# Kernel tuning notes

Measured on AMD Instinct MI355X. Metric: run time of the kernel, lower is better.

Reference implementation:

```python
import jax, jax.numpy as jnp
import numpy as np

C = 768
H = 12
B = 4
T = 16
K = 196


def _ln(x, g, b, eps=1e-5):
    mu = jnp.mean(x, axis=-1, keepdims=True)
    var = jnp.mean(jnp.square(x - mu), axis=-1, keepdims=True)
    return (x - mu) / jnp.sqrt(var + eps) * g + b


def _mha(x, Wq, bq, Wk, bk, Wv, bv):
    # x: [b, n, c]; standard multi-head attention, scale = head_dim**-0.5
    b, n, c = x.shape
    hd = c // H
    scale = hd ** -0.5
    def heads(y):
        return y.reshape(b, n, H, hd).transpose(0, 2, 1, 3)  # b h n d
    q = heads(x @ Wq + bq)
    k = heads(x @ Wk + bk)
    v = heads(x @ Wv + bv)
    a = jax.nn.softmax(jnp.einsum('bhqd,bhkd->bhqk', q, k) * scale, axis=-1)
    o = jnp.einsum('bhqk,bhkd->bhqd', a, v)
    return o.transpose(0, 2, 1, 3).reshape(b, n, c)


def setup_inputs() -> dict:
    key = jax.random.key(0)
    ks = jax.random.split(key, 8)
    M = T * K + 1
    w = lambda k, shape: jax.random.normal(k, shape, dtype=jnp.float32) * 0.02
    return {
        'x': jax.random.normal(ks[0], (B, M, C), dtype=jnp.float32),
        'ln1_g': jnp.ones((C,), jnp.float32), 'ln1_b': jnp.zeros((C,), jnp.float32),
        'tln_g': jnp.ones((C,), jnp.float32), 'tln_b': jnp.zeros((C,), jnp.float32),
        'ln2_g': jnp.ones((C,), jnp.float32), 'ln2_b': jnp.zeros((C,), jnp.float32),
        'Ws': w(ks[1], (4, C, C)), 'bs': jnp.zeros((4, C), jnp.float32),
        'Wt': w(ks[2], (9, C, C)), 'bt': jnp.zeros((9, C), jnp.float32),
        'Wtp': w(ks[3], (3, C, C)), 'btp': jnp.zeros((3, C), jnp.float32),
        'Wfc': w(ks[4], (C, C)), 'bfc': jnp.zeros((C,), jnp.float32),
        'W1': w(ks[5], (C, 4 * C)), 'b1': jnp.zeros((4 * C,), jnp.float32),
        'W2': w(ks[6], (4 * C, C)), 'b2': jnp.zeros((C,), jnp.float32),
        'T': T, 'K': K,
    }


def reference(x, ln1_g, ln1_b, tln_g, tln_b, ln2_g, ln2_b, Ws, bs, Wt, bt, Wtp, btp, Wfc, bfc, W1, b1, W2, b2, T, K):
    Bsz, M, Cd = x.shape
    t1, t2 = T // 4, T // 2
    # ---- temporal branch: 'b (k t) c -> (b k) t c' ----
    xt = x[:, 1:].reshape(Bsz * K, T, Cd)
    h = _ln(xt, tln_g, tln_b)
    # three windowed temporal scales
    o4 = _mha(h[:, T - t1:], Wt[0], bt[0], Wt[1], bt[1], Wt[2], bt[2])
    o8 = _mha(h[:, t2:], Wt[3], bt[3], Wt[4], bt[4], Wt[5], bt[5])
    o16 = _mha(h, Wt[6], bt[6], Wt[7], bt[7], Wt[8], bt[8])
    o4 = o4 @ Wtp[0] + btp[0]
    o8 = o8.at[:, t1:].set(0.5 * o8[:, t1:] + 0.5 * o4)
    o8 = o8 @ Wtp[1] + btp[1]
    o16 = o16.at[:, t2:].set(0.5 * o16[:, t2:] + 0.5 * o8)
    o16 = o16 @ Wtp[2] + btp[2]
    res_temporal = o16.reshape(Bsz, K * T, Cd)  # '(b k) t c -> b (k t) c'
    xt2 = res_temporal @ Wfc + bfc + x[:, 1:]
    # ---- spatial branch: 'b (k t) c -> (b t) k c' with cls prepended ----
    init_cls = x[:, :1]  # [B,1,C]
    cls = jnp.broadcast_to(init_cls, (Bsz, T, Cd)).reshape(Bsz * T, 1, Cd)
    xs = xt2.reshape(Bsz, K, T, Cd).transpose(0, 2, 1, 3).reshape(Bsz * T, K, Cd)
    xs = jnp.concatenate([cls, xs], axis=1)  # [(B T), K+1, C]
    hs = _ln(xs, ln1_g, ln1_b)
    os_ = _mha(hs, Ws[0], bs[0], Ws[1], bs[1], Ws[2], bs[2]) @ Ws[3] + bs[3]
    cls_out = os_[:, 0].reshape(Bsz, T, Cd).mean(axis=1, keepdims=True)
    res_spatial = os_[:, 1:].reshape(Bsz, T, K, Cd).transpose(0, 2, 1, 3).reshape(Bsz, K * T, Cd)
    xn = jnp.concatenate([init_cls, xt2], axis=1) + jnp.concatenate([cls_out, res_spatial], axis=1)
    # ---- MLP ----
    h2 = _ln(xn, ln2_g, ln2_b)
    mlp = jax.nn.gelu(h2 @ W1 + b1, approximate=False) @ W2 + b2
    return xn + mlp
```

## Files before the change

kernel.cpp:

```cpp
#include <hip/hip_runtime.h>

typedef unsigned short u16;
typedef unsigned int   u32;
typedef __attribute__((ext_vector_type(8))) __bf16 bf16x8;
typedef __attribute__((ext_vector_type(4))) float  f32x4;
typedef __attribute__((ext_vector_type(4))) u16    u16x4;

#define DEV __device__ __forceinline__

DEV float bf2f(u16 u){ union { u32 i; float f; } x; x.i = ((u32)u) << 16; return x.f; }
DEV u16 f2bf(float f){ union { float f; u32 i; } x; x.f = f;
  u32 r = x.i + 0x7fffu + ((x.i >> 16) & 1u); return (u16)(r >> 16); }

DEV void gload16(const void* g, void* l){
  __builtin_amdgcn_global_load_lds((const __attribute__((address_space(1))) void*)g,
                                   (__attribute__((address_space(3))) void*)l, 16, 0, 0);
}

__global__ __launch_bounds__(256)
void twt_k(const float* __restrict__ src, u16* __restrict__ dst, int R, int C){
  __shared__ float t[32][33];
  int tx = threadIdx.x & 31, ty = threadIdx.x >> 5;
  int c0 = blockIdx.x * 32, r0 = blockIdx.y * 32;
  #pragma unroll
  for (int i = 0; i < 4; i++)
    t[ty + i*8][tx] = src[(size_t)(r0 + ty + i*8) * C + c0 + tx];
  __syncthreads();
  #pragma unroll
  for (int i = 0; i < 4; i++)
    dst[(size_t)(c0 + ty + i*8) * R + r0 + tx] = f2bf(t[tx][ty + i*8]);
}

__global__ __launch_bounds__(256)
void twt17_k(const float* __restrict__ Ws, const float* __restrict__ Wt,
             const float* __restrict__ Wtp, const float* __restrict__ Wfc,
             u16* __restrict__ dst){
  __shared__ float t[32][33];
  int z = blockIdx.z;
  const float* src = (z < 4)  ? Ws  + (size_t)z * 589824
                   : (z < 13) ? Wt  + (size_t)(z-4) * 589824
                   : (z < 16) ? Wtp + (size_t)(z-13) * 589824
                   : Wfc;
  u16* d = dst + (size_t)z * 589824;
  int tx = threadIdx.x & 31, ty = threadIdx.x >> 5;
  int c0 = blockIdx.x * 32, r0 = blockIdx.y * 32;
  #pragma unroll
  for (int i = 0; i < 4; i++)
    t[ty + i*8][tx] = src[(size_t)(r0 + ty + i*8) * 768 + c0 + tx];
  __syncthreads();
  #pragma unroll
  for (int i = 0; i < 4; i++)
    d[(size_t)(c0 + ty + i*8) * 768 + r0 + tx] = f2bf(t[tx][ty + i*8]);
}

__global__ __launch_bounds__(256)
void cvt_k(const float* __restrict__ src, u16* __restrict__ dst){
  int i = (blockIdx.x * 256 + threadIdx.x) * 4;
  float4 f = *(const float4*)(src + i);
  u16x4 p; p[0] = f2bf(f.x); p[1] = f2bf(f.y); p[2] = f2bf(f.z); p[3] = f2bf(f.w);
  *(u16x4*)(dst + i) = p;
}

__global__ __launch_bounds__(256)
void bprep_k(const float* __restrict__ btp2, const u16* __restrict__ WfcT,
             const float* __restrict__ bfc, float* __restrict__ bprime,
             float* __restrict__ zb){
  int lane = threadIdx.x & 63;
  int n = blockIdx.x * 4 + (threadIdx.x >> 6);
  const u16* wr = WfcT + (size_t)n * 768 + lane * 12;
  const float* br = btp2 + lane * 12;
  float acc = 0.f;
  #pragma unroll
  for (int i = 0; i < 3; i++){
    u16x4 w = *(const u16x4*)(wr + i * 4);
    float4 b = *(const float4*)(br + i * 4);
    acc += bf2f(w[0]) * b.x + bf2f(w[1]) * b.y + bf2f(w[2]) * b.z + bf2f(w[3]) * b.w;
  }
  #pragma unroll
  for (int off = 32; off; off >>= 1) acc += __shfl_xor(acc, off);
  if (lane == 0){ bprime[n] = acc + bfc[n]; zb[n] = 0.f; }
}

__global__ void fillz_k(u32* __restrict__ p, long n){
  long i = (long)blockIdx.x * 256 + threadIdx.x;
  long stride = (long)gridDim.x * 256;
  for (; i < n; i += stride) p[i] = 0;
}

template<int GM>
__global__ __launch_bounds__(256)
void ln_k(const float* __restrict__ f0, const u16* __restrict__ b0_,
          const float* __restrict__ gw, const float* __restrict__ bw,
          u16* __restrict__ out){
  int lane = threadIdx.x & 63;
  int tok = blockIdx.x * 4 + (threadIdx.x >> 6);
  const float* fsrc = nullptr; const u16* bsrc = nullptr;
  bool bfp = false;
  if constexpr (GM == 0){
    int b = tok / 3136, m = tok - b * 3136;
    fsrc = f0 + ((size_t)b * 3137 + 1 + m) * 768;
  } else if constexpr (GM == 1){
    int s = tok / 197, j = tok - s * 197;
    int b = s >> 4, t = s & 15;
    if (j == 0) fsrc = f0 + (size_t)b * 3137 * 768;
    else { bfp = true; bsrc = b0_ + ((size_t)b * 3136 + (size_t)(j - 1) * 16 + t) * 768; }
  } else {
    fsrc = f0 + (size_t)tok * 768;
  }
  float v[12]; float s1 = 0.f, s2 = 0.f;
  if (!bfp){
    #pragma unroll
    for (int i = 0; i < 3; i++){
      float4 f = *(const float4*)(fsrc + i * 256 + lane * 4);
      v[i*4+0] = f.x; v[i*4+1] = f.y; v[i*4+2] = f.z; v[i*4+3] = f.w;
    }
  } else {
    #pragma unroll
    for (int i = 0; i < 3; i++){
      u16x4 p = *(const u16x4*)(bsrc + i * 256 + lane * 4);
      v[i*4+0] = bf2f(p[0]); v[i*4+1] = bf2f(p[1]); v[i*4+2] = bf2f(p[2]); v[i*4+3] = bf2f(p[3]);
    }
  }
  #pragma unroll
  for (int i = 0; i < 12; i++){ s1 += v[i]; s2 += v[i]*v[i]; }
  #pragma unroll
  for (int off = 32; off; off >>= 1){ s1 += __shfl_xor(s1, off); s2 += __shfl_xor(s2, off); }
  float mu = s1 * (1.f/768.f);
  float rstd = rsqrtf(s2 * (1.f/768.f) - mu*mu + 1e-5f);
  #pragma unroll
  for (int i = 0; i < 3; i++){
    int c = i * 256 + lane * 4;
    float4 g4 = *(const float4*)(gw + c);
    float4 b4 = *(const float4*)(bw + c);
    u16x4 pk;
    pk[0] = f2bf((v[i*4+0]-mu)*rstd*g4.x + b4.x);
    pk[1] = f2bf((v[i*4+1]-mu)*rstd*g4.y + b4.y);
    pk[2] = f2bf((v[i*4+2]-mu)*rstd*g4.z + b4.z);
    pk[3] = f2bf((v[i*4+3]-mu)*rstd*g4.w + b4.w);
    *(u16x4*)(out + (size_t)tok * 768 + c) = pk;
  }
}

template<int MODE, int BIG>
__global__ __launch_bounds__(BIG ? 512 : 256, 4)
void gemm_k(const u16* __restrict__ A, const u16* __restrict__ Bw,
            const float* __restrict__ bias, void* out,
            const void* aux1, void* aux2, int nbx,
            int M, int K, int lda, int ldo,
            int aTs, int aTf, int at0, int oTs, int oTf, int ot0){
  constexpr int BM = BIG ? 256 : 128;
  constexpr int THREADS = BIG ? 512 : 256;
  __shared__ u16 lA[2][BM * 32];
  __shared__ u16 lB[2][128 * 32];
  const int tid = threadIdx.x;

  const int nwg = (int)gridDim.x;
  int id = (int)blockIdx.x;
  int qc = nwg >> 3, rc = nwg & 7;
  int xcd = id & 7, off = id >> 3;
  int wg = (xcd < rc ? xcd * (qc + 1) : rc * (qc + 1) + (xcd - rc) * qc) + off;
  int by = wg / nbx;
  int bx = wg - by * nbx;
  const int m0 = by * BM, n0 = bx * 128;

  const int lane = tid & 63, widx = tid >> 6;
  const int g = lane >> 4, r16 = lane & 15;
  const int wm = widx >> 1, wn = widx & 1;

  const u16* ga0; const u16* ga1; const u16* gb0; const u16* gb1 = nullptr;
  u32 loA0, loA1, loB0, loB1 = 0;
  {
    int li = tid;
    int ar = m0 + (li >> 2); if (ar > M - 1) ar = M - 1;
    ar = (ar / aTs) * aTf + at0 + (ar % aTs);
    ga0 = A + (size_t)ar * lda + (li & 3) * 8;
    loA0 = li * 8;
    li = tid + THREADS;
    ar = m0 + (li >> 2); if (ar > M - 1) ar = M - 1;
    ar = (ar / aTs) * aTf + at0 + (ar % aTs);
    ga1 = A + (size_t)ar * lda + (li & 3) * 8;
    loA1 = li * 8;
    gb0 = Bw + (size_t)(n0 + (tid >> 2)) * K + (tid & 3) * 8;
    loB0 = tid * 8;
    if constexpr (!BIG){
      int lj = tid + 256;
      gb1 = Bw + (size_t)(n0 + (lj >> 2)) * K + (lj & 3) * 8;
      loB1 = lj * 8;
    }
  }

  const f32x4 vz = {0.f, 0.f, 0.f, 0.f};
  f32x4 acc[4][4];
  #pragma unroll
  for (int i = 0; i < 4; i++)
    #pragma unroll
    for (int j = 0; j < 4; j++) acc[i][j] = vz;

  const int kiter = K >> 5;

  gload16(ga0, &lA[0][loA0]);
  gload16(ga1, &lA[0][loA1]);
  gload16(gb0, &lB[0][loB0]);
  if constexpr (!BIG) gload16(gb1, &lB[0][loB1]);
  ga0 += 32; ga1 += 32; gb0 += 32;
  if constexpr (!BIG) gb1 += 32;
  __syncthreads();

  for (int kt = 0; kt < kiter; ++kt){
    const int cur = kt & 1;
    if (kt + 1 < kiter){
      const int nxt = cur ^ 1;
      gload16(ga0, &lA[nxt][loA0]);
      gload16(ga1, &lA[nxt][loA1]);
      gload16(gb0, &lB[nxt][loB0]);
      if constexpr (!BIG) gload16(gb1, &lB[nxt][loB1]);
      ga0 += 32; ga1 += 32; gb0 += 32;
      if constexpr (!BIG) gb1 += 32;
    }
    bf16x8 af[4], bfr[4];
    #pragma unroll
    for (int i = 0; i < 4; i++){
      af[i]  = *(const bf16x8*)(&lA[cur][(wm * 64 + i * 16 + r16) * 32 + g * 8]);
      bfr[i] = *(const bf16x8*)(&lB[cur][(wn * 64 + i * 16 + r16) * 32 + g * 8]);
    }
    #pragma unroll
    for (int i = 0; i < 4; i++)
      #pragma unroll
      for (int j = 0; j < 4; j++)
        acc[i][j] = __builtin_amdgcn_mfma_f32_16x16x32_bf16(af[i], bfr[j], acc[i][j], 0, 0, 0);
    __syncthreads();
  }

  #pragma unroll
  for (int i = 0; i < 4; i++){
    const int lrow = wm * 64 + i * 16 + g * 4;
    #pragma unroll
    for (int j = 0; j < 4; j++){
      const int Cg = n0 + wn * 64 + j * 16 + r16;
      const float b0 = bias[Cg];
      float vv[4];
      #pragma unroll
      for (int r = 0; r < 4; r++) vv[r] = acc[i][j][r] + b0;

      if constexpr (MODE == 8){
        int mat = Cg / 768, c0 = Cg - mat * 768;
        if (mat < 2){
          #pragma unroll
          for (int r = 0; r < 4; r++){
            int R = m0 + lrow + r;
            if (R < M)
              ((u16*)out)[(size_t)mat * ot0 * 768 + (size_t)R * 768 + c0] = f2bf(vv[r]);
          }
        } else {
          int R0 = m0 + lrow;
          if (R0 < M){
            int seq_ = R0 / oTs, t0 = R0 - seq_ * oTs;
            u16x4 pk;
            #pragma unroll
            for (int r = 0; r < 4; r++) pk[r] = f2bf(vv[r]);
            *(u16x4*)((u16*)aux2 +
              ((size_t)(seq_ * 12 + (c0 >> 6)) * 64 + (c0 & 63)) * ldo + t0) = pk;
          }
        }
      } else if constexpr (MODE == 9){
        int mat = Cg / 768, c0 = Cg - mat * 768;
        if (mat < 2){
          #pragma unroll
          for (int r = 0; r < 4; r++){
            int R = m0 + lrow + r;
            if (R < M)
              ((u16*)out)[(size_t)mat * ot0 * 768 + (size_t)R * 768 + c0] = f2bf(vv[r]);
          }
        } else {
          int R0 = m0 + lrow;
          if (R0 < M){
            int s_ = R0 / 197, j0 = R0 - s_ * 197;
            if (j0 <= 193){
              u16x4 pk;
              #pragma unroll
              for (int r = 0; r < 4; r++) pk[r] = f2bf(vv[r]);
              *(u16x4*)((u16*)aux2 +
                ((size_t)(s_ * 12 + (c0 >> 6)) * 64 + (c0 & 63)) * 224 + j0 + (s_ & 3)) = pk;
            } else {
              #pragma unroll
              for (int r = 0; r < 4; r++){
                int R = R0 + r;
                if (R < M){
                  int s2 = R / 197, j2 = R - s2 * 197;
                  ((u16*)aux2)[((size_t)(s2 * 12 + (c0 >> 6)) * 64 + (c0 & 63)) * 224
                               + j2 + (s2 & 3)] = f2bf(vv[r]);
                }
              }
            }
          }
        }
      } else {
        #pragma unroll
        for (int r = 0; r < 4; r++){
          const int R = m0 + lrow + r;
          if (R >= M) continue;
          float val = vv[r];
          if constexpr (MODE == 0){
            ((u16*)out)[(size_t)R * ldo + Cg] = f2bf(val);
          } else if constexpr (MODE == 1){
            int Ro = (R / oTs) * oTf + ot0 + (R % oTs);
            u16* po = (u16*)out + (size_t)Ro * ldo + Cg;
            *po = f2bf(0.5f * val + 0.5f * bf2f(*po));
          } else if constexpr (MODE == 2){
            int b_ = R / 3136, m_ = R - b_ * 3136;
            ((u16*)out)[(size_t)R * 768 + Cg] =
                f2bf(val + ((const float*)aux1)[((size_t)b_ * 3137 + 1 + m_) * 768 + Cg]);
          } else if constexpr (MODE == 3){
            int s_ = R / 197, j_ = R - s_ * 197;
            if (j_ == 0){
              ((float*)aux2)[(size_t)s_ * 768 + Cg] = val;
            } else {
              int b_ = s_ >> 4, t_ = s_ & 15, m_ = (j_ - 1) * 16 + t_;
              ((float*)out)[((size_t)b_ * 3137 + 1 + m_) * 768 + Cg] =
                  val + bf2f(((const u16*)aux1)[((size_t)b_ * 3136 + m_) * 768 + Cg]);
            }
          } else if constexpr (MODE == 4){
            float c = val * (0.7978845608f + 0.0356774081f * val * val);
            float e2 = __expf(2.f * fabsf(c));
            float th = __builtin_copysignf(1.f - 2.f / (e2 + 1.f), c);
            ((u16*)out)[(size_t)R * ldo + Cg] = f2bf(0.5f * val * (1.f + th));
          } else if constexpr (MODE == 5){
            ((float*)out)[(size_t)R * 768 + Cg] = val + ((const float*)aux1)[(size_t)R * 768 + Cg];
          }
        }
      }
    }
  }
}

template<int TS, int TSPAD>
__global__ __launch_bounds__(256)
void tattn_k(const u16* __restrict__ q, const u16* __restrict__ k,
             const u16* __restrict__ vt, u16* __restrict__ o){
  const int lane = threadIdx.x & 63;
  const int g = lane >> 4, r16 = lane & 15;
  int p = blockIdx.x * 4 + (threadIdx.x >> 6);
  int seq = p / 12, h = p - seq * 12;

  int trow = (TS < 16 && r16 >= TS) ? TS - 1 : r16;
  size_t qko = (size_t)(seq * TS + trow) * 768 + h * 64 + g * 8;
  bf16x8 ak0 = *(const bf16x8*)(k + qko);
  bf16x8 ak1 = *(const bf16x8*)(k + qko + 32);
  bf16x8 bq0 = *(const bf16x8*)(q + qko);
  bf16x8 bq1 = *(const bf16x8*)(q + qko + 32);

  f32x4 s = {0.f, 0.f, 0.f, 0.f};
  s = __builtin_amdgcn_mfma_f32_16x16x32_bf16(ak0, bq0, s, 0, 0, 0);
  s = __builtin_amdgcn_mfma_f32_16x16x32_bf16(ak1, bq1, s, 0, 0, 0);

  const float C = 0.125f * 1.44269504089f;
  float pv[4]; float mx = -3e38f;
  #pragma unroll
  for (int r = 0; r < 4; r++){
    float x = (g * 4 + r < TS) ? s[r] : -3e38f;
    pv[r] = x; mx = fmaxf(mx, x);
  }
  mx = fmaxf(mx, __shfl_xor(mx, 16));
  mx = fmaxf(mx, __shfl_xor(mx, 32));
  float sum = 0.f;
  #pragma unroll
  for (int r = 0; r < 4; r++){ pv[r] = exp2f((pv[r] - mx) * C); sum += pv[r]; }
  sum += __shfl_xor(sum, 16);
  sum += __shfl_xor(sum, 32);
  float inv = 1.f / sum;
  #pragma unroll
  for (int r = 0; r < 4; r++) pv[r] *= inv;

  u32 w0 = (u32)f2bf(pv[0]) | ((u32)f2bf(pv[1]) << 16);
  u32 w1 = (u32)f2bf(pv[2]) | ((u32)f2bf(pv[3]) << 16);
  int a0 = ((g * 2) * 16 + r16) * 4;
  int a1 = ((g * 2 + 1) * 16 + r16) * 4;
  u32 msk = (g < 2) ? 0xFFFFFFFFu : 0u;
  union { u32 w[4]; bf16x8 v; } pa;
  pa.w[0] = msk & (u32)__builtin_amdgcn_ds_bpermute(a0, (int)w0);
  pa.w[1] = msk & (u32)__builtin_amdgcn_ds_bpermute(a0, (int)w1);
  pa.w[2] = msk & (u32)__builtin_amdgcn_ds_bpermute(a1, (int)w0);
  pa.w[3] = msk & (u32)__builtin_amdgcn_ds_bpermute(a1, (int)w1);

  const u16* vb = vt + ((size_t)(seq * 12 + h) * 64) * TSPAD;
  const f32x4 vz = {0.f, 0.f, 0.f, 0.f};
  f32x4 oc[4];
  #pragma unroll
  for (int dt = 0; dt < 4; ++dt){
    bf16x8 bv = *(const bf16x8*)(vb + (size_t)(dt * 16 + r16) * TSPAD + g * 8);
    oc[dt] = __builtin_amdgcn_mfma_f32_16x16x32_bf16(pa.v, bv, vz, 0, 0, 0);
  }
  #pragma unroll
  for (int rr = 0; rr < 4; ++rr){
    int qr = g * 4 + rr;
    if (qr < TS){
      size_t ob = (size_t)(seq * TS + qr) * 768 + h * 64 + r16;
      #pragma unroll
      for (int dt = 0; dt < 4; ++dt)
        o[ob + dt * 16] = f2bf(oc[dt][rr]);
    }
  }
}

__global__ __launch_bounds__(256)
void sattn_k(const u16* __restrict__ qs, const u16* __restrict__ ks,
             const u16* __restrict__ vt, u16* __restrict__ o){
  __shared__ u16 PlAll[4][16 * 224];
  const int wid = threadIdx.x >> 6;
  u16* Pl = PlAll[wid];
  const int lane = threadIdx.x & 63;
  const int g = lane >> 4, r16 = lane & 15;
  int gi = blockIdx.x * 4 + wid;
  int chunk = gi % 13; int sh_ = gi / 13;
  int h = sh_ % 12, s = sh_ / 12;
  const int shft = s & 3;
  const float sc_l2e = 0.125f * 1.44269504089f;

  #pragma unroll
  for (int i = 0; i < 4; i++){
    Pl[(i * 4 + g) * 224 + 208 + r16] = 0;
    if (r16 < 4) Pl[(i * 4 + g) * 224 + r16] = 0;
  }

  int q0 = chunk * 16;
  int qrow = q0 + r16; if (qrow > 196) qrow = 196;
  const u16* qp = qs + ((size_t)(s * 197 + qrow)) * 768 + h * 64 + g * 8;
  bf16x8 aq0 = *(const bf16x8*)qp;
  bf16x8 aq1 = *(const bf16x8*)(qp + 32);

  f32x4 scv[13];
  #pragma unroll
  for (int jt = 0; jt < 13; ++jt){
    int krow = jt * 16 + r16; if (krow > 196) krow = 196;
    const u16* kp = ks + ((size_t)(s * 197 + krow)) * 768 + h * 64 + g * 8;
    bf16x8 b0 = *(const bf16x8*)kp;
    bf16x8 b1 = *(const bf16x8*)(kp + 32);
    f32x4 z = {0.f, 0.f, 0.f, 0.f};
    z = __builtin_amdgcn_mfma_f32_16x16x32_bf16(aq0, b0, z, 0, 0, 0);
    z = __builtin_amdgcn_mfma_f32_16x16x32_bf16(aq1, b1, z, 0, 0, 0);
    scv[jt] = z;
  }
  float mrow[4] = {-3e38f, -3e38f, -3e38f, -3e38f};
  #pragma unroll
  for (int jt = 0; jt < 13; ++jt)
    #pragma unroll
    for (int r = 0; r < 4; r++){
      float x = (jt * 16 + r16 < 197) ? scv[jt][r] : -3e38f;
      scv[jt][r] = x;
      mrow[r] = fmaxf(mrow[r], x);
    }
  #pragma unroll
  for (int off = 1; off < 16; off <<= 1)
    #pragma unroll
    for (int r = 0; r < 4; r++) mrow[r] = fmaxf(mrow[r], __shfl_xor(mrow[r], off));
  float srow[4] = {0.f, 0.f, 0.f, 0.f};
  #pragma unroll
  for (int jt = 0; jt < 13; ++jt)
    #pragma unroll
    for (int r = 0; r < 4; r++){
      float e = exp2f((scv[jt][r] - mrow[r]) * sc_l2e);
      scv[jt][r] = e;
      srow[r] += e;
    }
  #pragma unroll
  for (int off = 1; off < 16; off <<= 1)
    #pragma unroll
    for (int r = 0; r < 4; r++) srow[r] += __shfl_xor(srow[r], off);
  float inv[4];
  #pragma unroll
  for (int r = 0; r < 4; r++) inv[r] = 1.f / srow[r];
  #pragma unroll
  for (int jt = 0; jt < 13; ++jt)
    #pragma unroll
    for (int r = 0; r < 4; r++)
      Pl[(g * 4 + r) * 224 + jt * 16 + r16 + shft] = f2bf(scv[jt][r] * inv[r]);
  __syncthreads();
  const u16* vbase = vt + ((size_t)(s * 12 + h) * 64) * 224;
  f32x4 oc[4]; const f32x4 vz = {0.f,0.f,0.f,0.f};
  #pragma unroll
  for (int dt = 0; dt < 4; dt++) oc[dt] = vz;
  #pragma unroll
  for (int ks2 = 0; ks2 < 7; ++ks2){
    bf16x8 ap = *(const bf16x8*)(Pl + r16 * 224 + ks2 * 32 + g * 8);
    #pragma unroll
    for (int dt = 0; dt < 4; ++dt){
      const u16* vp = vbase + ((size_t)(dt * 16 + r16)) * 224 + ks2 * 32 + g * 8;
      bf16x8 bv = *(const bf16x8*)vp;
      oc[dt] = __builtin_amdgcn_mfma_f32_16x16x32_bf16(ap, bv, oc[dt], 0, 0, 0);
    }
  }
  #pragma unroll
  for (int dt = 0; dt < 4; ++dt)
    #pragma unroll
    for (int r = 0; r < 4; r++){
      int qr2 = q0 + g * 4 + r;
      if (qr2 < 197)
        o[((size_t)(s * 197 + qr2)) * 768 + h * 64 + dt * 16 + r16] = f2bf(oc[dt][r]);
    }
}

__global__ __launch_bounds__(256)
void clsfin_k(const float* __restrict__ x, const float* __restrict__ cb, float* __restrict__ xn){
  int b = blockIdx.x;
  int c = blockIdx.y * 256 + threadIdx.x;
  float s = 0.f;
  #pragma unroll
  for (int t = 0; t < 16; t++) s += cb[((size_t)(b * 16 + t)) * 768 + c];
  xn[(size_t)b * 3137 * 768 + c] = x[(size_t)b * 3137 * 768 + c] + s * (1.f / 16.f);
}

extern "C" void kernel_launch(void* const* d_in, const int* in_sizes, int n_in,
                              void* d_out, int out_size, void* d_ws, size_t ws_size,
                              hipStream_t stream){
  (void)in_sizes; (void)n_in; (void)out_size;
  const float* x    = (const float*)d_in[0];
  const float* ln1g = (const float*)d_in[1];
  const float* ln1b = (const float*)d_in[2];
  const float* tlng = (const float*)d_in[3];
  const float* tlnb = (const float*)d_in[4];
  const float* ln2g = (const float*)d_in[5];
  const float* ln2b = (const float*)d_in[6];
  const float* Ws   = (const float*)d_in[7];
  const float* bs   = (const float*)d_in[8];
  const float* Wt   = (const float*)d_in[9];
  const float* bt   = (const float*)d_in[10];
  const float* Wtp  = (const float*)d_in[11];
  const float* btp  = (const float*)d_in[12];
  const float* Wfc  = (const float*)d_in[13];
  const float* bfc  = (const float*)d_in[14];
  const float* W1   = (const float*)d_in[15];
  const float* b1   = (const float*)d_in[16];
  const float* W2   = (const float*)d_in[17];
  const float* b2   = (const float*)d_in[18];
  float* out = (float*)d_out;

  constexpr size_t MiB = 1048576;
  constexpr size_t C2  = 589824;
  constexpr size_t W_BYTES = (17 * C2 + 2 * 2359296) * 2;
  constexpr size_t NEED = W_BYTES + 143 * MiB;
  if (ws_size < NEED) return;

  char* wsb  = (char*)d_ws;
  u16*  wbuf = (u16*)wsb;
  u16*  W1T  = wbuf + 17 * C2;
  u16*  W2T  = W1T + (size_t)3072 * 768;
  char* A0   = wsb + W_BYTES;

  u16*  ht  = (u16*)(A0 + 0   * MiB);
  u16*  qk  = (u16*)(A0 + 20  * MiB);
  u16*  vtb = (u16*)(A0 + 58  * MiB);
  u16*  o16 = (u16*)(A0 + 86  * MiB);
  u16*  o8  = (u16*)(A0 + 105 * MiB);
  u16*  o4  = (u16*)(A0 + 115 * MiB);
  u16*  xt2 = (u16*)(A0 + 105 * MiB);
  float* xn = (float*)(A0 + 20 * MiB);
  u16*  wtp2b = (u16*)(A0 + 132 * MiB);
  u16*  WpT   = (u16*)(A0 + 134 * MiB);
  float* bprime = (float*)(A0 + 136 * MiB);
  float* zb     = bprime + 1024;
  float* clsb = (float*)(A0 + 142 * MiB);
  u16*  hs  = ht;  u16* osb = ht; u16* h2 = ht;
  u16*  a1  = (u16*)(A0 + 58 * MiB);

  twt17_k<<<dim3(24, 24, 17), 256, 0, stream>>>(Ws, Wt, Wtp, Wfc, wbuf);
  twt_k<<<dim3(96, 24), 256, 0, stream>>>(W1, W1T, 768, 3072);
  twt_k<<<dim3(24, 96), 256, 0, stream>>>(W2, W2T, 3072, 768);
  cvt_k<<<576, 256, 0, stream>>>(Wtp + 2 * 589824, wtp2b);
  bprep_k<<<192, 256, 0, stream>>>(btp + 1536, wbuf + 16*C2, bfc, bprime, zb);
  gemm_k<0,0><<<36, 256, 0, stream>>>(wbuf + 16*C2, wtp2b, zb, WpT, nullptr, nullptr, 6, 768, 768, 768, 768, 1,1,0, 1,1,0);

  ln_k<0><<<3136, 256, 0, stream>>>(x, nullptr, tlng, tlnb, ht);

  gemm_k<8,1><<<49*18, 512, 0, stream>>>(ht, wbuf + 10*C2, bt + 6*768, qk, nullptr, vtb, 18, 12544, 768, 768, 24, 1,1,0, 16,1,12544);
  tattn_k<16,24><<<2352, 256, 0, stream>>>(qk, qk + (size_t)12544*768, vtb, o16);

  gemm_k<8,0><<<49*18, 256, 0, stream>>>(ht, wbuf +  7*C2, bt + 3*768, qk, nullptr, vtb, 18, 6272, 768, 768, 16, 8,16,8, 8,1,6272);
  tattn_k< 8,16><<<2352, 256, 0, stream>>>(qk, qk + (size_t)6272*768, vtb, o8);

  gemm_k<8,0><<<25*18, 256, 0, stream>>>(ht, wbuf +  4*C2, bt + 0*768, qk, nullptr, vtb, 18, 3136, 768, 768, 16, 4,16,12, 4,1,3136);
  tattn_k< 4,16><<<2352, 256, 0, stream>>>(qk, qk + (size_t)3136*768, vtb, o4);

  gemm_k<1,0><<<25*6, 256, 0, stream>>>(o4,  wbuf + 13*C2, btp + 0,   o8,  nullptr, nullptr, 6, 3136, 768, 768, 768, 1,1,0, 4,8,4);
  gemm_k<1,0><<<49*6, 256, 0, stream>>>(o8,  wbuf + 14*C2, btp + 768, o16, nullptr, nullptr, 6, 6272, 768, 768, 768, 1,1,0, 8,16,8);
  gemm_k<2,0><<<98*6, 256, 0, stream>>>(o16, WpT,          bprime,    xt2, x, nullptr,       6, 12544, 768, 768, 768, 1,1,0, 1,1,0);

  ln_k<1><<<3152, 256, 0, stream>>>(x, xt2, ln1g, ln1b, hs);
  fillz_k<<<2048, 256, 0, stream>>>((u32*)vtb, 5505024);
  gemm_k<9,1><<<50*18, 512, 0, stream>>>(hs, wbuf + 0*C2, bs + 0, qk, nullptr, vtb, 18, 12608, 768, 768, 224, 1,1,0, 1,1,12608);

  sattn_k<<<2496, 256, 0, stream>>>(qk, qk + (size_t)12608*768, vtb, osb);

  gemm_k<3,0><<<99*6, 256, 0, stream>>>(osb, wbuf + 3*C2, bs + 2304, xn, xt2, clsb, 6, 12608, 768, 768, 768, 1,1,0, 1,1,0);
  clsfin_k<<<dim3(4, 3), 256, 0, stream>>>(x, clsb, xn);

  ln_k<2><<<3137, 256, 0, stream>>>(xn, nullptr, ln2g, ln2b, h2);
  gemm_k<4,1><<<50*24, 512, 0, stream>>>(h2, W1T, b1, a1,  nullptr, nullptr, 24, 12548, 768, 768, 3072, 1,1,0, 1,1,0);
  gemm_k<5,0><<<99*6, 256, 0, stream>>>(a1, W2T, b2, out, xn, nullptr,       6, 12548, 3072, 3072, 768, 1,1,0, 1,1,0);
}
```

Baseline: 710.4 us.

## Merge weight prep and temporal LN, fuse LN1 with zero-fill, store xn as bf16

Folds the four weight transpose/convert kernels and the temporal LayerNorm into one launch that dispatches on block index. It also merges the spatial LayerNorm with the V-buffer zero fill, which removes several kernel launches and tail gaps. The residual xn is now stored in bf16 instead of fp32, roughly halving its write and its two reads (LN2 and the final residual add). The cost is lower precision in the residual stream that feeds the output, and one bf16 rounding more before the MLP residual.

```diff
diff --git a/kernel.cpp b/kernel.cpp
--- a/kernel.cpp
+++ b/kernel.cpp
@@ -18,47 +18,81 @@
 }
 
 __global__ __launch_bounds__(256)
-void twt_k(const float* __restrict__ src, u16* __restrict__ dst, int R, int C){
+void wprep_k(const float* __restrict__ Ws, const float* __restrict__ Wt,
+             const float* __restrict__ Wtp, const float* __restrict__ Wfc,
+             u16* __restrict__ wbuf,
+             const float* __restrict__ W1, u16* __restrict__ W1T,
+             const float* __restrict__ W2, u16* __restrict__ W2T,
+             u16* __restrict__ wtp2b,
+             const float* __restrict__ x, const float* __restrict__ tlng,
+             const float* __restrict__ tlnb, u16* __restrict__ ht){
   __shared__ float t[32][33];
-  int tx = threadIdx.x & 31, ty = threadIdx.x >> 5;
-  int c0 = blockIdx.x * 32, r0 = blockIdx.y * 32;
-  #pragma unroll
-  for (int i = 0; i < 4; i++)
-    t[ty + i*8][tx] = src[(size_t)(r0 + ty + i*8) * C + c0 + tx];
-  __syncthreads();
-  #pragma unroll
-  for (int i = 0; i < 4; i++)
-    dst[(size_t)(c0 + ty + i*8) * R + r0 + tx] = f2bf(t[tx][ty + i*8]);
-}
-
-__global__ __launch_bounds__(256)
-void twt17_k(const float* __restrict__ Ws, const float* __restrict__ Wt,
-             const float* __restrict__ Wtp, const float* __restrict__ Wfc,
-             u16* __restrict__ dst){
-  __shared__ float t[32][33];
-  int z = blockIdx.z;
-  const float* src = (z < 4)  ? Ws  + (size_t)z * 589824
-                   : (z < 13) ? Wt  + (size_t)(z-4) * 589824
-                   : (z < 16) ? Wtp + (size_t)(z-13) * 589824
-                   : Wfc;
-  u16* d = dst + (size_t)z * 589824;
-  int tx = threadIdx.x & 31, ty = threadIdx.x >> 5;
-  int c0 = blockIdx.x * 32, r0 = blockIdx.y * 32;
-  #pragma unroll
-  for (int i = 0; i < 4; i++)
-    t[ty + i*8][tx] = src[(size_t)(r0 + ty + i*8) * 768 + c0 + tx];
-  __syncthreads();
-  #pragma unroll
-  for (int i = 0; i < 4; i++)
-    d[(size_t)(c0 + ty + i*8) * 768 + r0 + tx] = f2bf(t[tx][ty + i*8]);
-}
-
-__global__ __launch_bounds__(256)
-void cvt_k(const float* __restrict__ src, u16* __restrict__ dst){
-  int i = (blockIdx.x * 256 + threadIdx.x) * 4;
-  float4 f = *(const float4*)(src + i);
-  u16x4 p; p[0] = f2bf(f.x); p[1] = f2bf(f.y); p[2] = f2bf(f.z); p[3] = f2bf(f.w);
-  *(u16x4*)(dst + i) = p;
+  const int b = blockIdx.x, tid = threadIdx.x;
+  if (b < 9792){
+    int z = b / 576, r2 = b - z * 576;
+    int c0 = (r2 % 24) * 32, r0 = (r2 / 24) * 32;
+    const float* src = (z < 4)  ? Ws  + (size_t)z * 589824
+                     : (z < 13) ? Wt  + (size_t)(z-4) * 589824
+                     : (z < 16) ? Wtp + (size_t)(z-13) * 589824
+                     : Wfc;
+    u16* d = wbuf + (size_t)z * 589824;
+    int tx = tid & 31, ty = tid >> 5;
+    #pragma unroll
+    for (int i = 0; i < 4; i++)
+      t[ty + i*8][tx] = src[(size_t)(r0 + ty + i*8) * 768 + c0 + tx];
+    __syncthreads();
+    #pragma unroll
+    for (int i = 0; i < 4; i++)
+      d[(size_t)(c0 + ty + i*8) * 768 + r0 + tx] = f2bf(t[tx][ty + i*8]);
+  } else if (b < 14400){
+    const float* src; u16* dst; int R, C, bx, by;
+    if (b < 12096){ int r = b - 9792;  src = W1; dst = W1T; R = 768;  C = 3072; bx = r % 96; by = r / 96; }
+    else          { int r = b - 12096; src = W2; dst = W2T; R = 3072; C = 768;  bx = r % 24; by = r / 24; }
+    int c0 = bx * 32, r0 = by * 32;
+    int tx = tid & 31, ty = tid >> 5;
+    #pragma unroll
+    for (int i = 0; i < 4; i++)
+      t[ty + i*8][tx] = src[(size_t)(r0 + ty + i*8) * C + c0 + tx];
+    __syncthreads();
+    #pragma unroll
+    for (int i = 0; i < 4; i++)
+      dst[(size_t)(c0 + ty + i*8) * R + r0 + tx] = f2bf(t[tx][ty + i*8]);
+  } else if (b < 14976){
+    int i = ((b - 14400) * 256 + tid) * 4;
+    float4 f = *(const float4*)(Wtp + 2 * 589824 + i);
+    u16x4 p; p[0] = f2bf(f.x); p[1] = f2bf(f.y); p[2] = f2bf(f.z); p[3] = f2bf(f.w);
+    *(u16x4*)(wtp2b + i) = p;
+    (void)wtp2b;
+  } else {
+    int lane = tid & 63;
+    int tok = (b - 14976) * 4 + (tid >> 6);
+    int bb = tok / 3136, m = tok - bb * 3136;
+    const float* fsrc = x + ((size_t)bb * 3137 + 1 + m) * 768;
+    float v[12]; float s1 = 0.f, s2 = 0.f;
+    #pragma unroll
+    for (int i = 0; i < 3; i++){
+      float4 f = *(const float4*)(fsrc + i * 256 + lane * 4);
+      v[i*4+0] = f.x; v[i*4+1] = f.y; v[i*4+2] = f.z; v[i*4+3] = f.w;
+    }
+    #pragma unroll
+    for (int i = 0; i < 12; i++){ s1 += v[i]; s2 += v[i]*v[i]; }
+    #pragma unroll
+    for (int off = 32; off; off >>= 1){ s1 += __shfl_xor(s1, off); s2 += __shfl_xor(s2, off); }
+    float mu = s1 * (1.f/768.f);
+    float rstd = rsqrtf(s2 * (1.f/768.f) - mu*mu + 1e-5f);
+    #pragma unroll
+    for (int i = 0; i < 3; i++){
+      int c = i * 256 + lane * 4;
+      float4 g4 = *(const float4*)(tlng + c);
+      float4 b4 = *(const float4*)(tlnb + c);
+      u16x4 pk;
+      pk[0] = f2bf((v[i*4+0]-mu)*rstd*g4.x + b4.x);
+      pk[1] = f2bf((v[i*4+1]-mu)*rstd*g4.y + b4.y);
+      pk[2] = f2bf((v[i*4+2]-mu)*rstd*g4.z + b4.z);
+      pk[3] = f2bf((v[i*4+3]-mu)*rstd*g4.w + b4.w);
+      *(u16x4*)(ht + (size_t)tok * 768 + c) = pk;
+    }
+  }
 }
 
 __global__ __launch_bounds__(256)
@@ -81,45 +115,68 @@
   if (lane == 0){ bprime[n] = acc + bfc[n]; zb[n] = 0.f; }
 }
 
-__global__ void fillz_k(u32* __restrict__ p, long n){
-  long i = (long)blockIdx.x * 256 + threadIdx.x;
-  long stride = (long)gridDim.x * 256;
-  for (; i < n; i += stride) p[i] = 0;
-}
-
-template<int GM>
 __global__ __launch_bounds__(256)
-void ln_k(const float* __restrict__ f0, const u16* __restrict__ b0_,
-          const float* __restrict__ gw, const float* __restrict__ bw,
-          u16* __restrict__ out){
+void lnfz_k(const float* __restrict__ x, const u16* __restrict__ xt2,
+            const float* __restrict__ gw, const float* __restrict__ bw,
+            u16* __restrict__ out, u32* __restrict__ vzp, long nz){
+  int b = blockIdx.x;
+  if (b >= 3152){
+    long i = (long)(b - 3152) * 256 + threadIdx.x;
+    long stride = 2048L * 256;
+    for (; i < nz; i += stride) vzp[i] = 0;
+    return;
+  }
   int lane = threadIdx.x & 63;
-  int tok = blockIdx.x * 4 + (threadIdx.x >> 6);
-  const float* fsrc = nullptr; const u16* bsrc = nullptr;
-  bool bfp = false;
-  if constexpr (GM == 0){
-    int b = tok / 3136, m = tok - b * 3136;
-    fsrc = f0 + ((size_t)b * 3137 + 1 + m) * 768;
-  } else if constexpr (GM == 1){
-    int s = tok / 197, j = tok - s * 197;
-    int b = s >> 4, t = s & 15;
-    if (j == 0) fsrc = f0 + (size_t)b * 3137 * 768;
-    else { bfp = true; bsrc = b0_ + ((size_t)b * 3136 + (size_t)(j - 1) * 16 + t) * 768; }
-  } else {
-    fsrc = f0 + (size_t)tok * 768;
-  }
+  int tok = b * 4 + (threadIdx.x >> 6);
+  int s = tok / 197, j = tok - s * 197;
+  int bb = s >> 4, tt = s & 15;
   float v[12]; float s1 = 0.f, s2 = 0.f;
-  if (!bfp){
+  if (j == 0){
+    const float* fsrc = x + (size_t)bb * 3137 * 768;
     #pragma unroll
     for (int i = 0; i < 3; i++){
       float4 f = *(const float4*)(fsrc + i * 256 + lane * 4);
       v[i*4+0] = f.x; v[i*4+1] = f.y; v[i*4+2] = f.z; v[i*4+3] = f.w;
     }
   } else {
+    const u16* bsrc = xt2 + ((size_t)bb * 3136 + (size_t)(j - 1) * 16 + tt) * 768;
     #pragma unroll
     for (int i = 0; i < 3; i++){
       u16x4 p = *(const u16x4*)(bsrc + i * 256 + lane * 4);
       v[i*4+0] = bf2f(p[0]); v[i*4+1] = bf2f(p[1]); v[i*4+2] = bf2f(p[2]); v[i*4+3] = bf2f(p[3]);
     }
+  }
+  #pragma unroll
+  for (int i = 0; i < 12; i++){ s1 += v[i]; s2 += v[i]*v[i]; }
+  #pragma unroll
+  for (int off = 32; off; off >>= 1){ s1 += __shfl_xor(s1, off); s2 += __shfl_xor(s2, off); }
+  float mu = s1 * (1.f/768.f);
+  float rstd = rsqrtf(s2 * (1.f/768.f) - mu*mu + 1e-5f);
+  #pragma unroll
+  for (int i = 0; i < 3; i++){
+    int c = i * 256 + lane * 4;
+    float4 g4 = *(const float4*)(gw + c);
+    float4 b4 = *(const float4*)(bw + c);
+    u16x4 pk;
+    pk[0] = f2bf((v[i*4+0]-mu)*rstd*g4.x + b4.x);
+    pk[1] = f2bf((v[i*4+1]-mu)*rstd*g4.y + b4.y);
+    pk[2] = f2bf((v[i*4+2]-mu)*rstd*g4.z + b4.z);
+    pk[3] = f2bf((v[i*4+3]-mu)*rstd*g4.w + b4.w);
+    *(u16x4*)(out + (size_t)tok * 768 + c) = pk;
+  }
+}
+
+__global__ __launch_bounds__(256)
+void ln2_k(const u16* __restrict__ xnb, const float* __restrict__ gw,
+           const float* __restrict__ bw, u16* __restrict__ out){
+  int lane = threadIdx.x & 63;
+  int tok = blockIdx.x * 4 + (threadIdx.x >> 6);
+  const u16* bsrc = xnb + (size_t)tok * 768;
+  float v[12]; float s1 = 0.f, s2 = 0.f;
+  #pragma unroll
+  for (int i = 0; i < 3; i++){
+    u16x4 p = *(const u16x4*)(bsrc + i * 256 + lane * 4);
+    v[i*4+0] = bf2f(p[0]); v[i*4+1] = bf2f(p[1]); v[i*4+2] = bf2f(p[2]); v[i*4+3] = bf2f(p[3]);
   }
   #pragma unroll
   for (int i = 0; i < 12; i++){ s1 += v[i]; s2 += v[i]*v[i]; }
@@ -316,8 +373,8 @@
               ((float*)aux2)[(size_t)s_ * 768 + Cg] = val;
             } else {
               int b_ = s_ >> 4, t_ = s_ & 15, m_ = (j_ - 1) * 16 + t_;
-              ((float*)out)[((size_t)b_ * 3137 + 1 + m_) * 768 + Cg] =
-                  val + bf2f(((const u16*)aux1)[((size_t)b_ * 3136 + m_) * 768 + Cg]);
+              ((u16*)out)[((size_t)b_ * 3137 + 1 + m_) * 768 + Cg] =
+                  f2bf(val + bf2f(((const u16*)aux1)[((size_t)b_ * 3136 + m_) * 768 + Cg]));
             }
           } else if constexpr (MODE == 4){
             float c = val * (0.7978845608f + 0.0356774081f * val * val);
@@ -325,7 +382,8 @@
             float th = __builtin_copysignf(1.f - 2.f / (e2 + 1.f), c);
             ((u16*)out)[(size_t)R * ldo + Cg] = f2bf(0.5f * val * (1.f + th));
           } else if constexpr (MODE == 5){
-            ((float*)out)[(size_t)R * 768 + Cg] = val + ((const float*)aux1)[(size_t)R * 768 + Cg];
+            ((float*)out)[(size_t)R * 768 + Cg] =
+                val + bf2f(((const u16*)aux1)[(size_t)R * 768 + Cg]);
           }
         }
       }
@@ -500,13 +558,13 @@
 }
 
 __global__ __launch_bounds__(256)
-void clsfin_k(const float* __restrict__ x, const float* __restrict__ cb, float* __restrict__ xn){
+void clsfin_k(const float* __restrict__ x, const float* __restrict__ cb, u16* __restrict__ xn){
   int b = blockIdx.x;
   int c = blockIdx.y * 256 + threadIdx.x;
   float s = 0.f;
   #pragma unroll
   for (int t = 0; t < 16; t++) s += cb[((size_t)(b * 16 + t)) * 768 + c];
-  xn[(size_t)b * 3137 * 768 + c] = x[(size_t)b * 3137 * 768 + c] + s * (1.f / 16.f);
+  xn[(size_t)b * 3137 * 768 + c] = f2bf(x[(size_t)b * 3137 * 768 + c] + s * (1.f / 16.f));
 }
 
 extern "C" void kernel_launch(void* const* d_in, const int* in_sizes, int n_in,
@@ -553,7 +611,7 @@
   u16*  o8  = (u16*)(A0 + 105 * MiB);
   u16*  o4  = (u16*)(A0 + 115 * MiB);
   u16*  xt2 = (u16*)(A0 + 105 * MiB);
-  float* xn = (float*)(A0 + 20 * MiB);
+  u16*  xnb = (u16*)(A0 + 20 * MiB);
   u16*  wtp2b = (u16*)(A0 + 132 * MiB);
   u16*  WpT   = (u16*)(A0 + 134 * MiB);
   float* bprime = (float*)(A0 + 136 * MiB);
@@ -562,14 +620,10 @@
   u16*  hs  = ht;  u16* osb = ht; u16* h2 = ht;
   u16*  a1  = (u16*)(A0 + 58 * MiB);
 
-  twt17_k<<<dim3(24, 24, 17), 256, 0, stream>>>(Ws, Wt, Wtp, Wfc, wbuf);
-  twt_k<<<dim3(96, 24), 256, 0, stream>>>(W1, W1T, 768, 3072);
-  twt_k<<<dim3(24, 96), 256, 0, stream>>>(W2, W2T, 3072, 768);
-  cvt_k<<<576, 256, 0, stream>>>(Wtp + 2 * 589824, wtp2b);
+  wprep_k<<<18112, 256, 0, stream>>>(Ws, Wt, Wtp, Wfc, wbuf, W1, W1T, W2, W2T,
+                                     wtp2b, x, tlng, tlnb, ht);
   bprep_k<<<192, 256, 0, stream>>>(btp + 1536, wbuf + 16*C2, bfc, bprime, zb);
   gemm_k<0,0><<<36, 256, 0, stream>>>(wbuf + 16*C2, wtp2b, zb, WpT, nullptr, nullptr, 6, 768, 768, 768, 768, 1,1,0, 1,1,0);
-
-  ln_k<0><<<3136, 256, 0, stream>>>(x, nullptr, tlng, tlnb, ht);
 
   gemm_k<8,1><<<49*18, 512, 0, stream>>>(ht, wbuf + 10*C2, bt + 6*768, qk, nullptr, vtb, 18, 12544, 768, 768, 24, 1,1,0, 16,1,12544);
   tattn_k<16,24><<<2352, 256, 0, stream>>>(qk, qk + (size_t)12544*768, vtb, o16);
@@ -584,16 +638,15 @@
   gemm_k<1,0><<<49*6, 256, 0, stream>>>(o8,  wbuf + 14*C2, btp + 768, o16, nullptr, nullptr, 6, 6272, 768, 768, 768, 1,1,0, 8,16,8);
   gemm_k<2,0><<<98*6, 256, 0, stream>>>(o16, WpT,          bprime,    xt2, x, nullptr,       6, 12544, 768, 768, 768, 1,1,0, 1,1,0);
 
-  ln_k<1><<<3152, 256, 0, stream>>>(x, xt2, ln1g, ln1b, hs);
-  fillz_k<<<2048, 256, 0, stream>>>((u32*)vtb, 5505024);
+  lnfz_k<<<5200, 256, 0, stream>>>(x, xt2, ln1g, ln1b, hs, (u32*)vtb, 5505024);
   gemm_k<9,1><<<50*18, 512, 0, stream>>>(hs, wbuf + 0*C2, bs + 0, qk, nullptr, vtb, 18, 12608, 768, 768, 224, 1,1,0, 1,1,12608);
 
   sattn_k<<<2496, 256, 0, stream>>>(qk, qk + (size_t)12608*768, vtb, osb);
 
-  gemm_k<3,0><<<99*6, 256, 0, stream>>>(osb, wbuf + 3*C2, bs + 2304, xn, xt2, clsb, 6, 12608, 768, 768, 768, 1,1,0, 1,1,0);
-  clsfin_k<<<dim3(4, 3), 256, 0, stream>>>(x, clsb, xn);
-
-  ln_k<2><<<3137, 256, 0, stream>>>(xn, nullptr, ln2g, ln2b, h2);
+  gemm_k<3,0><<<99*6, 256, 0, stream>>>(osb, wbuf + 3*C2, bs + 2304, xnb, xt2, clsb, 6, 12608, 768, 768, 768, 1,1,0, 1,1,0);
+  clsfin_k<<<dim3(4, 3), 256, 0, stream>>>(x, clsb, xnb);
+
+  ln2_k<<<3137, 256, 0, stream>>>(xnb, ln2g, ln2b, h2);
   gemm_k<4,1><<<50*24, 512, 0, stream>>>(h2, W1T, b1, a1,  nullptr, nullptr, 24, 12548, 768, 768, 3072, 1,1,0, 1,1,0);
-  gemm_k<5,0><<<99*6, 256, 0, stream>>>(a1, W2T, b2, out, xn, nullptr,       6, 12548, 3072, 3072, 768, 1,1,0, 1,1,0);
-}
+  gemm_k<5,0><<<99*6, 256, 0, stream>>>(a1, W2T, b2, out, xnb, nullptr,      6, 12548, 3072, 3072, 768, 1,1,0, 1,1,0);
+}
```

Result: faster. 696.3 us (-2.0%).
